# Optimization experiments

Hardware: AMD Instinct MI355X
Metric: run time of the kernel (lower is better)

## Reference

```python
import jax, jax.numpy as jnp
import numpy as np

SHORT = 2000
CUTVALS = [0, 2000, 12000, 40000, 100000]  # [0] + cutoffs + [n_classes]
OSZ = [10000, 28000, 60000]
HSZ = [384, 192, 96]
IN_F = 768
LN_EPS = 1e-5


def setup_inputs() -> dict:
    key = jax.random.key(0)
    ks = jax.random.split(key, 16)
    B, L = 256, 20
    inp = {
        "x": jax.random.normal(ks[0], (B, IN_F), jnp.float32),
        "head_W": jax.random.normal(ks[1], (SHORT + 3, IN_F), jnp.float32) / np.sqrt(IN_F),
        "target": jax.random.randint(ks[2], (B, L), 0, CUTVALS[-1], jnp.int64)
        if jax.config.jax_enable_x64 else jax.random.randint(ks[2], (B, L), 0, CUTVALS[-1], jnp.int32),
    }
    for i in range(3):
        inp[f"w1_{i}"] = jax.random.normal(ks[3 + 4 * i], (HSZ[i], IN_F), jnp.float32) / np.sqrt(IN_F)
        inp[f"g{i}"] = jnp.ones((HSZ[i],), jnp.float32)
        inp[f"b{i}"] = jnp.zeros((HSZ[i],), jnp.float32)
        inp[f"w2_{i}"] = jax.random.normal(ks[4 + 4 * i], (OSZ[i], HSZ[i]), jnp.float32) / np.sqrt(HSZ[i])
    return inp


def _bce_with_logits(logits, y):
    # matches torch BCEWithLogitsLoss(reduction='none')
    return jnp.maximum(logits, 0.0) - logits * y + jnp.log1p(jnp.exp(-jnp.abs(logits)))


def reference(x, head_W, w1_0, g0, b0, w2_0, w1_1, g1, b1, w2_1, w1_2, g2, b2, w2_2, target):
    W1, G, Bp, W2 = [w1_0, w1_1, w1_2], [g0, g1, g2], [b0, b1, b2], [w2_0, w2_1, w2_2]
    B = x.shape[0]
    rows = jnp.arange(B)[:, None]
    dt = x.dtype

    head_logits = x @ head_W.T  # [B, SHORT + n_clusters]

    # shortlist multi-hot (rows with no shortlist label stay all-zero, as in torch)
    m0 = target < SHORT
    onehot_short = jnp.zeros((B, SHORT), dt).at[rows, jnp.clip(target, 0, SHORT - 1)].max(m0.astype(dt))

    total_cluster = jnp.zeros((B,), dt)
    actives = []
    for i in range(3):
        low, high = CUTVALS[i + 1], CUTVALS[i + 2]
        osz = high - low
        m = (target >= low) & (target < high)  # [B, L]
        active = m.any(axis=1).astype(dt)      # [B]
        actives.append(active)
        # multi-hot targets for this cluster
        y = jnp.zeros((B, osz), dt).at[rows, jnp.clip(target - low, 0, osz - 1)].max(m.astype(dt))
        # tail projection: Linear -> LayerNorm -> ReLU -> Linear
        h = x @ W1[i].T
        mu = h.mean(-1, keepdims=True)
        var = ((h - mu) ** 2).mean(-1, keepdims=True)
        h = jax.nn.relu((h - mu) * jax.lax.rsqrt(var + LN_EPS) * G[i] + Bp[i])
        # p = sigmoid(cluster-root logit) * sigmoid(tail logits)
        root = jax.nn.sigmoid(head_logits[:, SHORT + i])[:, None]  # [B,1]
        p = root * jax.nn.sigmoid(h @ W2[i].T)                     # [B, osz]
        # torch BCELoss clamps log at -100
        bce = -(y * jnp.maximum(jnp.log(p), -100.0) + (1.0 - y) * jnp.maximum(jnp.log1p(-p), -100.0))
        total_cluster = total_cluster + active * bce.sum(axis=1)

    cluster_onehot = jnp.stack(actives, axis=1)  # [B, 3]
    head_y = jnp.concatenate([onehot_short, cluster_onehot], axis=1)
    head_loss = _bce_with_logits(head_logits, head_y)  # [B, SHORT+3]
    mult = (cluster_onehot == 0).astype(dt)
    head_loss = jnp.concatenate([head_loss[:, :SHORT], head_loss[:, SHORT:] * mult], axis=1)
    head_loss = head_loss.sum(axis=1)

    csz = jnp.asarray(OSZ, dt)
    num_loss = (mult + cluster_onehot * csz).sum(axis=1) + SHORT
    return ((head_loss + total_cluster) / num_loss).mean()
```

## Files before the change

### kernel.cpp

```cpp
#include <hip/hip_runtime.h>
#include <hip/hip_bf16.h>

#define INF 768
#define NSHORT 2000
#define NHEAD 2003

typedef __attribute__((ext_vector_type(8))) short  s16x8;
typedef __attribute__((ext_vector_type(4))) float  f32x4;
typedef __attribute__((ext_vector_type(8))) float  f32x8;

__device__ __forceinline__ float sigf(float z) { return 1.f / (1.f + __expf(-z)); }
__device__ __forceinline__ float softplusf(float z) {
    return fmaxf(z, 0.f) + __logf(1.f + __expf(-fabsf(z)));
}
__device__ __forceinline__ float qreduce16(float v) {
    v += __shfl_xor(v, 1); v += __shfl_xor(v, 2);
    v += __shfl_xor(v, 4); v += __shfl_xor(v, 8);
    return v;
}
__device__ __forceinline__ float wreduce64(float v) {
    v += __shfl_xor(v, 1);  v += __shfl_xor(v, 2);  v += __shfl_xor(v, 4);
    v += __shfl_xor(v, 8);  v += __shfl_xor(v, 16); v += __shfl_xor(v, 32);
    return v;
}
__device__ __forceinline__ short bfc(float x) {
    union { __hip_bfloat16 h; short s; } u; u.h = __float2bfloat16(x); return u.s;
}

template <int K32, int MODE, int AF32>
__device__ __forceinline__ void core_s(
    const void* __restrict__ Av, int ldA, int kbase,
    const float* __restrict__ W, int Kfull, int N, int stripe,
    short* __restrict__ lds,
    float* __restrict__ outH, int ldH,
    float* __restrict__ part, int pslot,
    const float* __restrict__ rootlogit, int ci)
{
    const int t = threadIdx.x;
    const int wave = t >> 6, lane = t & 63;
    const int quad = lane >> 4, l16 = lane & 15;
    const int rtb = wave * 4;

    {
        const int ct = t >> 6, l = t & 63;
        int col = stripe * 64 + ct * 16 + (l & 15);
        if (col >= N) col = N - 1;
        const float* src = W + (size_t)col * Kfull + kbase + (l >> 4) * 8;
        short* dst = lds + ((size_t)ct * 64 + l) * 8;
#pragma unroll
        for (int s = 0; s < K32; s++) {
            const f32x8 v = *(const f32x8*)(src + s * 32);
            s16x8 o;
#pragma unroll
            for (int i = 0; i < 8; i++) o[i] = bfc(v[i]);
            *(s16x8*)(dst + (size_t)s * 2048) = o;
        }
    }

    s16x8 af[2][4];
    const float* axp[4];
    const short* app[4];
    if (AF32) {
#pragma unroll
        for (int rt = 0; rt < 4; rt++) {
            axp[rt] = (const float*)Av + (size_t)((rtb + rt) * 16 + l16) * ldA + kbase + quad * 8;
            const f32x8 v = *(const f32x8*)(axp[rt]);
#pragma unroll
            for (int i = 0; i < 8; i++) af[0][rt][i] = bfc(v[i]);
        }
    } else {
#pragma unroll
        for (int rt = 0; rt < 4; rt++) {
            app[rt] = (const short*)Av + ((size_t)(rtb + rt) * ldA * 64 + lane) * 8;
            af[0][rt] = *(const s16x8*)(app[rt]);
        }
    }

    __syncthreads();

    const short* wbase = lds + (size_t)lane * 8;
    s16x8 wf[2][4];
#pragma unroll
    for (int ct = 0; ct < 4; ct++)
        wf[0][ct] = *(const s16x8*)(wbase + (size_t)ct * 512);

    f32x4 acc[4][4];
#pragma unroll
    for (int rt = 0; rt < 4; rt++)
#pragma unroll
        for (int ct = 0; ct < 4; ct++) acc[rt][ct] = (f32x4){0.f, 0.f, 0.f, 0.f};

#pragma unroll
    for (int j = 0; j < K32; j++) {
        const int b = j & 1, nb = b ^ 1;
        if (j + 1 < K32) {
            if (AF32) {
#pragma unroll
                for (int rt = 0; rt < 4; rt++) {
                    const f32x8 v = *(const f32x8*)(axp[rt] + (size_t)(j + 1) * 32);
#pragma unroll
                    for (int i = 0; i < 8; i++) af[nb][rt][i] = bfc(v[i]);
                }
            } else {
#pragma unroll
                for (int rt = 0; rt < 4; rt++)
                    af[nb][rt] = *(const s16x8*)(app[rt] + (size_t)(j + 1) * 512);
            }
#pragma unroll
            for (int ct = 0; ct < 4; ct++)
                wf[nb][ct] = *(const s16x8*)(wbase + (size_t)(j + 1) * 2048 + ct * 512);
        }
#pragma unroll
        for (int rt = 0; rt < 4; rt++)
#pragma unroll
            for (int ct = 0; ct < 4; ct++)
                acc[rt][ct] = __builtin_amdgcn_mfma_f32_16x16x32_bf16(
                    af[b][rt], wf[b][ct], acc[rt][ct], 0, 0, 0);
    }

    const int col0 = stripe * 64;
    if (MODE == 0) {
#pragma unroll
        for (int rt = 0; rt < 4; rt++)
#pragma unroll
            for (int ct = 0; ct < 4; ct++) {
                const int col = col0 + ct * 16 + l16;
                if (col < N) {
#pragma unroll
                    for (int r = 0; r < 4; r++)
                        outH[(size_t)((rtb + rt) * 16 + quad * 4 + r) * ldH + col] =
                            acc[rt][ct][r];
                }
            }
    } else {
#pragma unroll
        for (int rt = 0; rt < 4; rt++) {
#pragma unroll
            for (int r = 0; r < 4; r++) {
                const int row = (rtb + rt) * 16 + quad * 4 + r;
                const float rv = sigf(rootlogit[row * 3 + ci]);
                float pd = 1.f, pn = 1.f;
#pragma unroll
                for (int ct = 0; ct < 4; ct++) {
                    const int col = col0 + ct * 16 + l16;
                    const float tv = fminf(__expf(-acc[rt][ct][r]), 1e6f);
                    const float d = (col < N) ? (1.f + tv) : 1.f;
                    const float n = (col < N) ? (1.f + tv - rv) : 1.f;
                    pd *= d; pn *= n;
                }
                float s = __logf(pd) - __logf(pn);
                s = qreduce16(s);
                if (l16 == 0) part[(size_t)pslot * 256 + row] = s;
            }
        }
    }
}

__global__ __launch_bounds__(256, 3) void k_mm1(
    const float* __restrict__ x, const float* __restrict__ headW,
    const float* __restrict__ w10, const float* __restrict__ w11,
    const float* __restrict__ w12,
    float* zA, float* zB,
    float* h0a, float* h0b, float* h1a, float* h1b, float* h2a, float* h2b,
    float* __restrict__ rootlogit)
{
    __shared__ __align__(16) short smem[64 * 12 * 32];
    const int bx = blockIdx.x;
    if (bx < 64) {
        const int stripe = bx >> 1, kq = bx & 1;
        core_s<12, 0, 1>(x, INF, kq * 384, headW, INF, NHEAD, stripe, smem,
                         kq ? zB : zA, 2048, nullptr, 0, nullptr, 0);
    } else if (bx < 76) {
        const int m = bx - 64, stripe = m >> 1, kq = m & 1;
        core_s<12, 0, 1>(x, INF, kq * 384, w10, INF, 384, stripe, smem,
                         kq ? h0b : h0a, 384, nullptr, 0, nullptr, 0);
    } else if (bx < 82) {
        const int m = bx - 76, stripe = m >> 1, kq = m & 1;
        core_s<12, 0, 1>(x, INF, kq * 384, w11, INF, 192, stripe, smem,
                         kq ? h1b : h1a, 192, nullptr, 0, nullptr, 0);
    } else if (bx < 86) {
        const int m = bx - 82, stripe = m >> 1, kq = m & 1;
        core_s<12, 0, 1>(x, INF, kq * 384, w12, INF, 96, stripe, smem,
                         kq ? h2b : h2a, 96, nullptr, 0, nullptr, 0);
    } else {
        const int row = bx - 86, wave = threadIdx.x >> 6, lane = threadIdx.x & 63;
        if (wave < 3) {
            const float* xr = x + row * INF;
            const float* wr = headW + (size_t)(NSHORT + wave) * INF;
            float s = 0.f;
            for (int k = lane; k < INF; k += 64) s += xr[k] * wr[k];
            s = wreduce64(s);
            if (lane == 0) rootlogit[row * 3 + wave] = s;
        }
    }
}

__global__ __launch_bounds__(256) void k_ln(const float* h0a, const float* h0b,
                                            const float* h1a, const float* h1b,
                                            const float* h2a, const float* h2b,
                                            const float* g0, const float* g1, const float* g2,
                                            const float* b0, const float* b1, const float* b2,
                                            const float* zA, const float* zB,
                                            __hip_bfloat16* f0, __hip_bfloat16* f1,
                                            __hip_bfloat16* f2,
                                            __hip_bfloat16* p0, __hip_bfloat16* p1,
                                            __hip_bfloat16* p2,
                                            float* __restrict__ phead) {
    const int bx = blockIdx.x;
    if (bx < 192) {
        const int task = bx * 4 + (threadIdx.x >> 6);
        const int ci = task >> 8, row = task & 255, lane = threadIdx.x & 63;
        const float *ha, *hb, *g, *bb; __hip_bfloat16 *fo, *po; int hsz, K32;
        if (ci == 0)      { ha = h0a; hb = h0b; g = g0; bb = b0; fo = f0; po = p0; hsz = 384; K32 = 12; }
        else if (ci == 1) { ha = h1a; hb = h1b; g = g1; bb = b1; fo = f1; po = p1; hsz = 192; K32 = 6; }
        else              { ha = h2a; hb = h2b; g = g2; bb = b2; fo = f2; po = p2; hsz = 96;  K32 = 3; }
        const float* hra = ha + row * hsz;
        const float* hrb = hb + row * hsz;
        float s = 0.f, s2 = 0.f;
        for (int k = lane; k < hsz; k += 64) {
            const float v = hra[k] + hrb[k]; s += v; s2 += v * v;
        }
        s = wreduce64(s); s2 = wreduce64(s2);
        const float mu = s / hsz;
        const float var = s2 / hsz - mu * mu;
        const float rsn = rsqrtf(var + 1e-5f);
        const int nch = hsz >> 3;
        if (lane < nch) {
            const f32x8 va = *(const f32x8*)(hra + lane * 8);
            const f32x8 vb = *(const f32x8*)(hrb + lane * 8);
            const f32x8 gg = *(const f32x8*)(g + lane * 8);
            const f32x8 bv = *(const f32x8*)(bb + lane * 8);
            s16x8 o;
#pragma unroll
            for (int i = 0; i < 8; i++)
                o[i] = bfc(fmaxf((va[i] + vb[i] - mu) * rsn * gg[i] + bv[i], 0.f));
            *(s16x8*)((short*)fo + (size_t)row * hsz + lane * 8) = o;
            const size_t chunk = ((size_t)(row >> 4) * K32 + (lane >> 2)) * 64
                               + (lane & 3) * 16 + (row & 15);
            *(s16x8*)((short*)po + chunk * 8) = o;
        }
    } else {
        const int row = bx - 192, t = threadIdx.x;
        const int wave = t >> 6, lane = t & 63;
        float val = 0.f;
        if (t < 250) {
            const f32x8 a = *(const f32x8*)(zA + (size_t)row * 2048 + t * 8);
            const f32x8 b = *(const f32x8*)(zB + (size_t)row * 2048 + t * 8);
            float m = 0.f, P = 1.f;
#pragma unroll
            for (int i = 0; i < 8; i++) {
                const float z = a[i] + b[i];
                m += fmaxf(z, 0.f);
                P *= 1.f + __expf(-fabsf(z));
            }
            val = m + __logf(P);
        }
        val = wreduce64(val);
        __shared__ float red[4];
        if (lane == 0) red[wave] = val;
        __syncthreads();
        if (t == 0) phead[row] = red[0] + red[1] + red[2] + red[3];
    }
}

__global__ __launch_bounds__(256, 3) void k_bce(const __hip_bfloat16* p0,
                                                const __hip_bfloat16* p1,
                                                const __hip_bfloat16* p2,
                                                const float* __restrict__ w20,
                                                const float* __restrict__ w21,
                                                const float* __restrict__ w22,
                                                float* __restrict__ part,
                                                const float* __restrict__ rootlogit) {
    __shared__ __align__(16) short smem[64 * 12 * 32];
    const int s = blockIdx.x;
    if (s < 157)
        core_s<12, 2, 0>(p0, 12, 0, w20, 384, 10000, s, smem,
                         nullptr, 0, part, s, rootlogit, 0);
    else if (s < 595)
        core_s<6, 2, 0>(p1, 6, 0, w21, 192, 28000, s - 157, smem,
                        nullptr, 0, part, s, rootlogit, 1);
    else
        core_s<3, 2, 0>(p2, 3, 0, w22, 96, 60000, s - 595, smem,
                        nullptr, 0, part, s, rootlogit, 2);
}

__global__ __launch_bounds__(256) void k_red(const float* __restrict__ part,
                                             const float* __restrict__ phead,
                                             const float* __restrict__ rootlogit,
                                             const int* __restrict__ target,
                                             const float* __restrict__ x,
                                             const float* __restrict__ headW,
                                             const __hip_bfloat16* f0,
                                             const __hip_bfloat16* f1,
                                             const __hip_bfloat16* f2,
                                             const float* w20, const float* w21, const float* w22,
                                             float* __restrict__ out) {
    const int row = blockIdx.x;
    const int t = threadIdx.x, wave = t >> 6, lane = t & 63;
    __shared__ float sx[INF];
    __shared__ __hip_bfloat16 shb[384 + 192 + 96];
    __shared__ int st[20];
    __shared__ float scorr[4];
    __shared__ float red[4][4];
    for (int i = t; i < INF; i += 256) sx[i] = x[row * INF + i];
    for (int i = t; i < 384; i += 256) shb[i] = f0[row * 384 + i];
    for (int i = t; i < 192; i += 256) shb[384 + i] = f1[row * 192 + i];
    for (int i = t; i < 96; i += 256)  shb[576 + i] = f2[row * 96 + i];
    if (t < 20) st[t] = target[row * 20 + t];
    if (t < 4) scorr[t] = 0.f;
    __syncthreads();
    for (int l = wave; l < 20; l += 4) {
        const int tg = st[l];
        bool dup = false;
        for (int m = 0; m < l; m++) dup |= (st[m] == tg);
        if (dup) continue;
        if (tg < NSHORT) {
            const float* wr = headW + (size_t)tg * INF;
            float z = 0.f;
            for (int k = lane; k < INF; k += 64) z += sx[k] * wr[k];
            z = wreduce64(z);
            if (lane == 0) atomicAdd(&scorr[3], -z);
        } else {
            int ci, low, hsz, hoff; const float* w2;
            if (tg < 12000)      { ci = 0; low = 2000;  hsz = 384; hoff = 0;   w2 = w20; }
            else if (tg < 40000) { ci = 1; low = 12000; hsz = 192; hoff = 384; w2 = w21; }
            else                 { ci = 2; low = 40000; hsz = 96;  hoff = 576; w2 = w22; }
            const float* wr = w2 + (size_t)(tg - low) * hsz;
            float z = 0.f;
            for (int k = lane; k < hsz; k += 64)
                z += __bfloat162float(shb[hoff + k]) * wr[k];
            z = wreduce64(z);
            if (lane == 0) {
                const float rvv = sigf(rootlogit[row * 3 + ci]);
                const float p = rvv * sigf(z);
                atomicAdd(&scorr[ci],
                          -fmaxf(__logf(p), -100.f) + fmaxf(__logf(1.f - p), -100.f));
            }
        }
    }
    float c0 = 0.f, c1 = 0.f, c2 = 0.f;
    for (int i = t; i < 1533; i += 256) {
        const float v = part[(size_t)i * 256 + row];
        if (i < 157) c0 += v; else if (i < 595) c1 += v; else c2 += v;
    }
    c0 = wreduce64(c0); c1 = wreduce64(c1); c2 = wreduce64(c2);
    if (lane == 0) { red[0][wave] = c0; red[1][wave] = c1; red[2][wave] = c2; }
    __syncthreads();
    if (t == 0) {
        float cc[3];
        for (int i = 0; i < 3; i++) cc[i] = red[i][0] + red[i][1] + red[i][2] + red[i][3];
        float hsum = phead[row] + scorr[3];
        bool act[3] = {false, false, false};
        for (int l = 0; l < 20; l++) {
            const int tg = target[row * 20 + l];
            if (tg >= 2000) {
                if (tg < 12000) act[0] = true;
                else if (tg < 40000) act[1] = true;
                else act[2] = true;
            }
        }
        float total = 0.f, num = 2000.f;
        const float csz[3] = {10000.f, 28000.f, 60000.f};
        for (int i = 0; i < 3; i++) {
            if (act[i]) { total += cc[i] + scorr[i]; num += csz[i]; }
            else        { hsum += softplusf(rootlogit[row * 3 + i]); num += 1.f; }
        }
        atomicAdd(out, (hsum + total) / num * (1.f / 256.f));
    }
}

extern "C" void kernel_launch(void* const* d_in, const int* in_sizes, int n_in,
                              void* d_out, int out_size, void* d_ws, size_t ws_size,
                              hipStream_t stream) {
    const float* x      = (const float*)d_in[0];
    const float* headW  = (const float*)d_in[1];
    const int*   target = (const int*)d_in[2];
    const float* w10 = (const float*)d_in[3];
    const float* g0  = (const float*)d_in[4];
    const float* b0  = (const float*)d_in[5];
    const float* w20 = (const float*)d_in[6];
    const float* w11 = (const float*)d_in[7];
    const float* g1  = (const float*)d_in[8];
    const float* b1  = (const float*)d_in[9];
    const float* w21 = (const float*)d_in[10];
    const float* w12 = (const float*)d_in[11];
    const float* g2  = (const float*)d_in[12];
    const float* b2  = (const float*)d_in[13];
    const float* w22 = (const float*)d_in[14];
    float* out = (float*)d_out;

    char* ws = (char*)d_ws;
    size_t off = 0;
    auto carve = [&](size_t bytes) -> void* {
        void* p = ws + off;
        off += (bytes + 255) & ~(size_t)255;
        return p;
    };
    float* zA            = (float*)carve((size_t)256 * 2048 * 4);
    float* zB            = (float*)carve((size_t)256 * 2048 * 4);
    float* h0a           = (float*)carve((size_t)256 * 384 * 4);
    float* h0b           = (float*)carve((size_t)256 * 384 * 4);
    float* h1a           = (float*)carve((size_t)256 * 192 * 4);
    float* h1b           = (float*)carve((size_t)256 * 192 * 4);
    float* h2a           = (float*)carve((size_t)256 * 96 * 4);
    float* h2b           = (float*)carve((size_t)256 * 96 * 4);
    __hip_bfloat16* f0   = (__hip_bfloat16*)carve((size_t)256 * 384 * 2);
    __hip_bfloat16* f1   = (__hip_bfloat16*)carve((size_t)256 * 192 * 2);
    __hip_bfloat16* f2   = (__hip_bfloat16*)carve((size_t)256 * 96 * 2);
    __hip_bfloat16* p0   = (__hip_bfloat16*)carve((size_t)256 * 384 * 2);
    __hip_bfloat16* p1   = (__hip_bfloat16*)carve((size_t)256 * 192 * 2);
    __hip_bfloat16* p2   = (__hip_bfloat16*)carve((size_t)256 * 96 * 2);
    float* rootlogit     = (float*)carve((size_t)256 * 3 * 4);
    float* phead         = (float*)carve((size_t)256 * 4);
    float* part          = (float*)carve((size_t)1536 * 256 * 4);

    hipMemsetAsync(out, 0, sizeof(float), stream);

    k_mm1<<<342, 256, 0, stream>>>(x, headW, w10, w11, w12,
                                   zA, zB, h0a, h0b, h1a, h1b, h2a, h2b, rootlogit);
    k_ln<<<448, 256, 0, stream>>>(h0a, h0b, h1a, h1b, h2a, h2b,
                                  g0, g1, g2, b0, b1, b2, zA, zB,
                                  f0, f1, f2, p0, p1, p2, phead);
    k_bce<<<1533, 256, 0, stream>>>(p0, p1, p2, w20, w21, w22, part, rootlogit);
    k_red<<<256, 256, 0, stream>>>(part, phead, rootlogit, target, x, headW,
                                   f0, f1, f2, w20, w21, w22, out);

    (void)in_sizes; (void)n_in; (void)out_size; (void)ws_size;
}
```

Before: 187.5 us.

## Chunk and double-buffer weight staging in GEMM core, raise split-K to four

The GEMM core now stages weights into LDS in small K-chunks with a double buffer, prefetching the next chunk's global loads while the current chunk runs MFMAs, instead of loading the whole K slice up front. This shrinks LDS use so more blocks can be resident, and k_bce's occupancy hint is raised. The first GEMM kernel splits K four ways instead of two, giving more blocks, and the layernorm kernel sums four partials. The output memset is folded into k_ln. The cost is extra partial-sum traffic, more syncs per block, and register pressure from holding prefetched fp32 chunks.

New measurement: 182.3 us. 1.03x faster.

```diff
diff --git a/kernel.cpp b/kernel.cpp
--- a/kernel.cpp
+++ b/kernel.cpp
@@ -27,63 +27,45 @@
     union { __hip_bfloat16 h; short s; } u; u.h = __float2bfloat16(x); return u.s;
 }
 
-template <int K32, int MODE, int AF32>
-__device__ __forceinline__ void core_s(
-    const void* __restrict__ Av, int ldA, int kbase,
+template <int K32, int KC, int MODE, int AF32>
+__device__ __forceinline__ void core_c(
+    const void* __restrict__ Av, int kbase32,
     const float* __restrict__ W, int Kfull, int N, int stripe,
     short* __restrict__ lds,
     float* __restrict__ outH, int ldH,
     float* __restrict__ part, int pslot,
     const float* __restrict__ rootlogit, int ci)
 {
+    constexpr int NCH = K32 / KC;
     const int t = threadIdx.x;
     const int wave = t >> 6, lane = t & 63;
     const int quad = lane >> 4, l16 = lane & 15;
     const int rtb = wave * 4;
 
-    {
-        const int ct = t >> 6, l = t & 63;
-        int col = stripe * 64 + ct * 16 + (l & 15);
-        if (col >= N) col = N - 1;
-        const float* src = W + (size_t)col * Kfull + kbase + (l >> 4) * 8;
-        short* dst = lds + ((size_t)ct * 64 + l) * 8;
-#pragma unroll
-        for (int s = 0; s < K32; s++) {
-            const f32x8 v = *(const f32x8*)(src + s * 32);
-            s16x8 o;
-#pragma unroll
-            for (int i = 0; i < 8; i++) o[i] = bfc(v[i]);
-            *(s16x8*)(dst + (size_t)s * 2048) = o;
-        }
-    }
-
-    s16x8 af[2][4];
-    const float* axp[4];
-    const short* app[4];
-    if (AF32) {
-#pragma unroll
-        for (int rt = 0; rt < 4; rt++) {
-            axp[rt] = (const float*)Av + (size_t)((rtb + rt) * 16 + l16) * ldA + kbase + quad * 8;
-            const f32x8 v = *(const f32x8*)(axp[rt]);
-#pragma unroll
-            for (int i = 0; i < 8; i++) af[0][rt][i] = bfc(v[i]);
-        }
-    } else {
-#pragma unroll
-        for (int rt = 0; rt < 4; rt++) {
-            app[rt] = (const short*)Av + ((size_t)(rtb + rt) * ldA * 64 + lane) * 8;
-            af[0][rt] = *(const s16x8*)(app[rt]);
-        }
-    }
-
+    const int sct = t >> 6, sl = t & 63;
+    int scol = stripe * 64 + sct * 16 + (sl & 15);
+    if (scol >= N) scol = N - 1;
+    const float* wsrc = W + (size_t)scol * Kfull + kbase32 * 32 + (sl >> 4) * 8;
+
+    size_t aoff[4];
+#pragma unroll
+    for (int rt = 0; rt < 4; rt++) {
+        if (AF32)
+            aoff[rt] = (size_t)((rtb + rt) * 16 + l16) * Kfull + kbase32 * 32 + quad * 8;
+        else
+            aoff[rt] = (size_t)(rtb + rt) * K32 * 512 + (size_t)lane * 8;
+    }
+
+#pragma unroll
+    for (int s = 0; s < KC; s++) {
+        const f32x8 v = *(const f32x8*)(wsrc + (size_t)s * 32);
+        s16x8 o;
+#pragma unroll
+        for (int i = 0; i < 8; i++) o[i] = bfc(v[i]);
+        *(s16x8*)(lds + (((size_t)s * 4 + sct) * 64 + sl) * 8) = o;
+    }
     __syncthreads();
 
-    const short* wbase = lds + (size_t)lane * 8;
-    s16x8 wf[2][4];
-#pragma unroll
-    for (int ct = 0; ct < 4; ct++)
-        wf[0][ct] = *(const s16x8*)(wbase + (size_t)ct * 512);
-
     f32x4 acc[4][4];
 #pragma unroll
     for (int rt = 0; rt < 4; rt++)
@@ -91,31 +73,50 @@
         for (int ct = 0; ct < 4; ct++) acc[rt][ct] = (f32x4){0.f, 0.f, 0.f, 0.f};
 
 #pragma unroll
-    for (int j = 0; j < K32; j++) {
-        const int b = j & 1, nb = b ^ 1;
-        if (j + 1 < K32) {
+    for (int c = 0; c < NCH; c++) {
+        short* lbuf = lds + (size_t)(c & 1) * (KC * 2048);
+        f32x8 nv[KC];
+        if (c + 1 < NCH) {
+#pragma unroll
+            for (int s = 0; s < KC; s++)
+                nv[s] = *(const f32x8*)(wsrc + ((size_t)((c + 1) * KC + s)) * 32);
+        }
+#pragma unroll
+        for (int jj = 0; jj < KC; jj++) {
+            const int jg = c * KC + jj;
+            s16x8 af[4];
             if (AF32) {
 #pragma unroll
                 for (int rt = 0; rt < 4; rt++) {
-                    const f32x8 v = *(const f32x8*)(axp[rt] + (size_t)(j + 1) * 32);
-#pragma unroll
-                    for (int i = 0; i < 8; i++) af[nb][rt][i] = bfc(v[i]);
+                    const f32x8 v = *(const f32x8*)((const float*)Av + aoff[rt] + (size_t)jg * 32);
+#pragma unroll
+                    for (int i = 0; i < 8; i++) af[rt][i] = bfc(v[i]);
                 }
             } else {
 #pragma unroll
                 for (int rt = 0; rt < 4; rt++)
-                    af[nb][rt] = *(const s16x8*)(app[rt] + (size_t)(j + 1) * 512);
-            }
-#pragma unroll
-            for (int ct = 0; ct < 4; ct++)
-                wf[nb][ct] = *(const s16x8*)(wbase + (size_t)(j + 1) * 2048 + ct * 512);
-        }
-#pragma unroll
-        for (int rt = 0; rt < 4; rt++)
-#pragma unroll
-            for (int ct = 0; ct < 4; ct++)
-                acc[rt][ct] = __builtin_amdgcn_mfma_f32_16x16x32_bf16(
-                    af[b][rt], wf[b][ct], acc[rt][ct], 0, 0, 0);
+                    af[rt] = *(const s16x8*)((const short*)Av + aoff[rt] + (size_t)jg * 512);
+            }
+#pragma unroll
+            for (int ct = 0; ct < 4; ct++) {
+                const s16x8 wf = *(const s16x8*)(lbuf + (((size_t)jj * 4 + ct) * 64 + lane) * 8);
+#pragma unroll
+                for (int rt = 0; rt < 4; rt++)
+                    acc[rt][ct] = __builtin_amdgcn_mfma_f32_16x16x32_bf16(
+                        af[rt], wf, acc[rt][ct], 0, 0, 0);
+            }
+        }
+        if (c + 1 < NCH) {
+            short* nbuf = lds + (size_t)((c + 1) & 1) * (KC * 2048);
+#pragma unroll
+            for (int s = 0; s < KC; s++) {
+                s16x8 o;
+#pragma unroll
+                for (int i = 0; i < 8; i++) o[i] = bfc(nv[s][i]);
+                *(s16x8*)(nbuf + (((size_t)s * 4 + sct) * 64 + sl) * 8) = o;
+            }
+            __syncthreads();
+        }
     }
 
     const int col0 = stripe * 64;
@@ -156,34 +157,43 @@
     }
 }
 
-__global__ __launch_bounds__(256, 3) void k_mm1(
+__global__ __launch_bounds__(256, 2) void k_mm1(
     const float* __restrict__ x, const float* __restrict__ headW,
     const float* __restrict__ w10, const float* __restrict__ w11,
     const float* __restrict__ w12,
-    float* zA, float* zB,
-    float* h0a, float* h0b, float* h1a, float* h1b, float* h2a, float* h2b,
+    float* __restrict__ zbase,
+    float* __restrict__ h0base,
+    float* __restrict__ h1base,
+    float* __restrict__ h2base,
     float* __restrict__ rootlogit)
 {
-    __shared__ __align__(16) short smem[64 * 12 * 32];
+    __shared__ __align__(16) short smem[8192];
     const int bx = blockIdx.x;
-    if (bx < 64) {
-        const int stripe = bx >> 1, kq = bx & 1;
-        core_s<12, 0, 1>(x, INF, kq * 384, headW, INF, NHEAD, stripe, smem,
-                         kq ? zB : zA, 2048, nullptr, 0, nullptr, 0);
-    } else if (bx < 76) {
-        const int m = bx - 64, stripe = m >> 1, kq = m & 1;
-        core_s<12, 0, 1>(x, INF, kq * 384, w10, INF, 384, stripe, smem,
-                         kq ? h0b : h0a, 384, nullptr, 0, nullptr, 0);
-    } else if (bx < 82) {
-        const int m = bx - 76, stripe = m >> 1, kq = m & 1;
-        core_s<12, 0, 1>(x, INF, kq * 384, w11, INF, 192, stripe, smem,
-                         kq ? h1b : h1a, 192, nullptr, 0, nullptr, 0);
-    } else if (bx < 86) {
-        const int m = bx - 82, stripe = m >> 1, kq = m & 1;
-        core_s<12, 0, 1>(x, INF, kq * 384, w12, INF, 96, stripe, smem,
-                         kq ? h2b : h2a, 96, nullptr, 0, nullptr, 0);
+    if (bx < 128) {
+        const int stripe = bx >> 2, kq = bx & 3;
+        core_c<6, 2, 0, 1>(x, kq * 6, headW, INF, NHEAD, stripe, smem,
+                           zbase + (size_t)kq * 256 * 2048, 2048,
+                           nullptr, 0, nullptr, 0);
+    } else if (bx < 172) {
+        const int m = bx - 128;
+        if (m < 24) {
+            const int stripe = m >> 2, kq = m & 3;
+            core_c<6, 2, 0, 1>(x, kq * 6, w10, INF, 384, stripe, smem,
+                               h0base + (size_t)kq * 256 * 384, 384,
+                               nullptr, 0, nullptr, 0);
+        } else if (m < 36) {
+            const int m2 = m - 24, stripe = m2 >> 2, kq = m2 & 3;
+            core_c<6, 2, 0, 1>(x, kq * 6, w11, INF, 192, stripe, smem,
+                               h1base + (size_t)kq * 256 * 192, 192,
+                               nullptr, 0, nullptr, 0);
+        } else {
+            const int m2 = m - 36, stripe = m2 >> 2, kq = m2 & 3;
+            core_c<6, 2, 0, 1>(x, kq * 6, w12, INF, 96, stripe, smem,
+                               h2base + (size_t)kq * 256 * 96, 96,
+                               nullptr, 0, nullptr, 0);
+        }
     } else {
-        const int row = bx - 86, wave = threadIdx.x >> 6, lane = threadIdx.x & 63;
+        const int row = bx - 172, wave = threadIdx.x >> 6, lane = threadIdx.x & 63;
         if (wave < 3) {
             const float* xr = x + row * INF;
             const float* wr = headW + (size_t)(NSHORT + wave) * INF;
@@ -195,30 +205,33 @@
     }
 }
 
-__global__ __launch_bounds__(256) void k_ln(const float* h0a, const float* h0b,
-                                            const float* h1a, const float* h1b,
-                                            const float* h2a, const float* h2b,
+__global__ __launch_bounds__(256) void k_ln(const float* __restrict__ h0base,
+                                            const float* __restrict__ h1base,
+                                            const float* __restrict__ h2base,
                                             const float* g0, const float* g1, const float* g2,
                                             const float* b0, const float* b1, const float* b2,
-                                            const float* zA, const float* zB,
+                                            const float* __restrict__ zbase,
                                             __hip_bfloat16* f0, __hip_bfloat16* f1,
                                             __hip_bfloat16* f2,
                                             __hip_bfloat16* p0, __hip_bfloat16* p1,
                                             __hip_bfloat16* p2,
-                                            float* __restrict__ phead) {
+                                            float* __restrict__ phead,
+                                            float* __restrict__ out) {
     const int bx = blockIdx.x;
+    if (bx == 0 && threadIdx.x == 0) out[0] = 0.f;
     if (bx < 192) {
         const int task = bx * 4 + (threadIdx.x >> 6);
         const int ci = task >> 8, row = task & 255, lane = threadIdx.x & 63;
-        const float *ha, *hb, *g, *bb; __hip_bfloat16 *fo, *po; int hsz, K32;
-        if (ci == 0)      { ha = h0a; hb = h0b; g = g0; bb = b0; fo = f0; po = p0; hsz = 384; K32 = 12; }
-        else if (ci == 1) { ha = h1a; hb = h1b; g = g1; bb = b1; fo = f1; po = p1; hsz = 192; K32 = 6; }
-        else              { ha = h2a; hb = h2b; g = g2; bb = b2; fo = f2; po = p2; hsz = 96;  K32 = 3; }
-        const float* hra = ha + row * hsz;
-        const float* hrb = hb + row * hsz;
+        const float *hb, *g, *bb; __hip_bfloat16 *fo, *po; int hsz, K32;
+        if (ci == 0)      { hb = h0base; g = g0; bb = b0; fo = f0; po = p0; hsz = 384; K32 = 12; }
+        else if (ci == 1) { hb = h1base; g = g1; bb = b1; fo = f1; po = p1; hsz = 192; K32 = 6; }
+        else              { hb = h2base; g = g2; bb = b2; fo = f2; po = p2; hsz = 96;  K32 = 3; }
+        const size_t qs = (size_t)256 * hsz;
+        const float* hr = hb + (size_t)row * hsz;
         float s = 0.f, s2 = 0.f;
         for (int k = lane; k < hsz; k += 64) {
-            const float v = hra[k] + hrb[k]; s += v; s2 += v * v;
+            const float v = hr[k] + hr[qs + k] + hr[2 * qs + k] + hr[3 * qs + k];
+            s += v; s2 += v * v;
         }
         s = wreduce64(s); s2 = wreduce64(s2);
         const float mu = s / hsz;
@@ -226,14 +239,18 @@
         const float rsn = rsqrtf(var + 1e-5f);
         const int nch = hsz >> 3;
         if (lane < nch) {
-            const f32x8 va = *(const f32x8*)(hra + lane * 8);
-            const f32x8 vb = *(const f32x8*)(hrb + lane * 8);
+            f32x8 v = *(const f32x8*)(hr + lane * 8);
+            const f32x8 v1 = *(const f32x8*)(hr + qs + lane * 8);
+            const f32x8 v2 = *(const f32x8*)(hr + 2 * qs + lane * 8);
+            const f32x8 v3 = *(const f32x8*)(hr + 3 * qs + lane * 8);
             const f32x8 gg = *(const f32x8*)(g + lane * 8);
             const f32x8 bv = *(const f32x8*)(bb + lane * 8);
             s16x8 o;
 #pragma unroll
-            for (int i = 0; i < 8; i++)
-                o[i] = bfc(fmaxf((va[i] + vb[i] - mu) * rsn * gg[i] + bv[i], 0.f));
+            for (int i = 0; i < 8; i++) {
+                const float hv = v[i] + v1[i] + v2[i] + v3[i];
+                o[i] = bfc(fmaxf((hv - mu) * rsn * gg[i] + bv[i], 0.f));
+            }
             *(s16x8*)((short*)fo + (size_t)row * hsz + lane * 8) = o;
             const size_t chunk = ((size_t)(row >> 4) * K32 + (lane >> 2)) * 64
                                + (lane & 3) * 16 + (row & 15);
@@ -244,12 +261,15 @@
         const int wave = t >> 6, lane = t & 63;
         float val = 0.f;
         if (t < 250) {
-            const f32x8 a = *(const f32x8*)(zA + (size_t)row * 2048 + t * 8);
-            const f32x8 b = *(const f32x8*)(zB + (size_t)row * 2048 + t * 8);
+            const size_t base = (size_t)row * 2048 + t * 8;
+            const f32x8 a = *(const f32x8*)(zbase + base);
+            const f32x8 b = *(const f32x8*)(zbase + 524288 + base);
+            const f32x8 c = *(const f32x8*)(zbase + 2 * 524288 + base);
+            const f32x8 d = *(const f32x8*)(zbase + 3 * 524288 + base);
             float m = 0.f, P = 1.f;
 #pragma unroll
             for (int i = 0; i < 8; i++) {
-                const float z = a[i] + b[i];
+                const float z = a[i] + b[i] + c[i] + d[i];
                 m += fmaxf(z, 0.f);
                 P *= 1.f + __expf(-fabsf(z));
             }
@@ -263,7 +283,7 @@
     }
 }
 
-__global__ __launch_bounds__(256, 3) void k_bce(const __hip_bfloat16* p0,
+__global__ __launch_bounds__(256, 4) void k_bce(const __hip_bfloat16* p0,
                                                 const __hip_bfloat16* p1,
                                                 const __hip_bfloat16* p2,
                                                 const float* __restrict__ w20,
@@ -271,17 +291,17 @@
                                                 const float* __restrict__ w22,
                                                 float* __restrict__ part,
                                                 const float* __restrict__ rootlogit) {
-    __shared__ __align__(16) short smem[64 * 12 * 32];
+    __shared__ __align__(16) short smem[8192];
     const int s = blockIdx.x;
     if (s < 157)
-        core_s<12, 2, 0>(p0, 12, 0, w20, 384, 10000, s, smem,
-                         nullptr, 0, part, s, rootlogit, 0);
+        core_c<12, 2, 2, 0>(p0, 0, w20, 384, 10000, s, smem,
+                            nullptr, 0, part, s, rootlogit, 0);
     else if (s < 595)
-        core_s<6, 2, 0>(p1, 6, 0, w21, 192, 28000, s - 157, smem,
-                        nullptr, 0, part, s, rootlogit, 1);
+        core_c<6, 2, 2, 0>(p1, 0, w21, 192, 28000, s - 157, smem,
+                           nullptr, 0, part, s, rootlogit, 1);
     else
-        core_s<3, 2, 0>(p2, 3, 0, w22, 96, 60000, s - 595, smem,
-                        nullptr, 0, part, s, rootlogit, 2);
+        core_c<3, 3, 2, 0>(p2, 0, w22, 96, 60000, s - 595, smem,
+                           nullptr, 0, part, s, rootlogit, 2);
 }
 
 __global__ __launch_bounds__(256) void k_red(const float* __restrict__ part,
@@ -396,14 +416,10 @@
         off += (bytes + 255) & ~(size_t)255;
         return p;
     };
-    float* zA            = (float*)carve((size_t)256 * 2048 * 4);
-    float* zB            = (float*)carve((size_t)256 * 2048 * 4);
-    float* h0a           = (float*)carve((size_t)256 * 384 * 4);
-    float* h0b           = (float*)carve((size_t)256 * 384 * 4);
-    float* h1a           = (float*)carve((size_t)256 * 192 * 4);
-    float* h1b           = (float*)carve((size_t)256 * 192 * 4);
-    float* h2a           = (float*)carve((size_t)256 * 96 * 4);
-    float* h2b           = (float*)carve((size_t)256 * 96 * 4);
+    float* zbase         = (float*)carve((size_t)4 * 256 * 2048 * 4);
+    float* h0base        = (float*)carve((size_t)4 * 256 * 384 * 4);
+    float* h1base        = (float*)carve((size_t)4 * 256 * 192 * 4);
+    float* h2base        = (float*)carve((size_t)4 * 256 * 96 * 4);
     __hip_bfloat16* f0   = (__hip_bfloat16*)carve((size_t)256 * 384 * 2);
     __hip_bfloat16* f1   = (__hip_bfloat16*)carve((size_t)256 * 192 * 2);
     __hip_bfloat16* f2   = (__hip_bfloat16*)carve((size_t)256 * 96 * 2);
@@ -414,13 +430,11 @@
     float* phead         = (float*)carve((size_t)256 * 4);
     float* part          = (float*)carve((size_t)1536 * 256 * 4);
 
-    hipMemsetAsync(out, 0, sizeof(float), stream);
-
-    k_mm1<<<342, 256, 0, stream>>>(x, headW, w10, w11, w12,
-                                   zA, zB, h0a, h0b, h1a, h1b, h2a, h2b, rootlogit);
-    k_ln<<<448, 256, 0, stream>>>(h0a, h0b, h1a, h1b, h2a, h2b,
-                                  g0, g1, g2, b0, b1, b2, zA, zB,
-                                  f0, f1, f2, p0, p1, p2, phead);
+    k_mm1<<<428, 256, 0, stream>>>(x, headW, w10, w11, w12,
+                                   zbase, h0base, h1base, h2base, rootlogit);
+    k_ln<<<448, 256, 0, stream>>>(h0base, h1base, h2base,
+                                  g0, g1, g2, b0, b1, b2, zbase,
+                                  f0, f1, f2, p0, p1, p2, phead, out);
     k_bce<<<1533, 256, 0, stream>>>(p0, p1, p2, w20, w21, w22, part, rootlogit);
     k_red<<<256, 256, 0, stream>>>(part, phead, rootlogit, target, x, headW,
                                    f0, f1, f2, w20, w21, w22, out);
```
